# Performance work log

Hardware: AMD Instinct MI355X
Metric: run time of the kernel (lower is better)

Reference implementation:

```python
import jax, jax.numpy as jnp
import numpy as np

B = 262144          # batch
D = 128             # in_dim == out_dim
BS = 16             # block size
K = 8               # number of blocks
RANK = 4            # low-rank blocks' rank
DENSE = np.array([0, 3, 6])   # block ids with mode 'dense'
DIAG = np.array([1, 4, 7])    # block ids with mode 'diagonal'
LR = np.array([2, 5])         # block ids with mode 'lowrank'
EPS = 1e-8


def setup_inputs() -> dict:
    key = jax.random.key(0)
    k1, k2, k3, k4, k5 = jax.random.split(key, 5)
    x = jax.random.normal(k1, (B, D), dtype=jnp.float32)
    # dense blocks: torch init is identity (d_in==d_out); add noise so math is non-trivial
    W_dense = jnp.eye(BS, dtype=jnp.float32)[None] + 0.1 * jax.random.normal(k2, (len(DENSE), BS, BS), dtype=jnp.float32)
    # diagonal blocks: torch init is ones; perturb slightly
    s_diag = 1.0 + 0.1 * jax.random.normal(k3, (len(DIAG), BS), dtype=jnp.float32)
    # lowrank blocks: xavier-uniform-like scale
    lim = float(np.sqrt(6.0 / (BS + RANK)))
    U = jax.random.uniform(k4, (len(LR), BS, RANK), dtype=jnp.float32, minval=-lim, maxval=lim)
    V = jax.random.uniform(k5, (len(LR), BS, RANK), dtype=jnp.float32, minval=-lim, maxval=lim)
    return {"x": x, "W_dense": W_dense, "s_diag": s_diag, "U": U, "V": V}


def reference(x, W_dense, s_diag, U, V):
    # blocks are contiguous [16*j, 16*(j+1)), so gather == reshape to [B, K, BS]
    x3 = x.reshape(B, K, BS)
    # dense blocks: torch Linear y = x @ W.T, W is [d_out, d_in]
    yd = jnp.einsum('bkd,kod->bko', x3[:, DENSE], W_dense)
    # diagonal blocks: elementwise scale
    yg = x3[:, DIAG] * s_diag
    # lowrank blocks: x @ V @ U.T
    yl = jnp.einsum('bkr,kor->bko', jnp.einsum('bkd,kdr->bkr', x3[:, LR], V), U)
    y = jnp.zeros_like(x3).at[:, DENSE].set(yd).at[:, DIAG].set(yg).at[:, LR].set(yl)
    y = y.reshape(B, D)
    # l2 normalize (normalize=True)
    norm = jnp.linalg.norm(y, axis=-1, keepdims=True)
    return y / (norm + EPS)
```

## Files before the change

kernel.cpp:

```cpp
#include <hip/hip_runtime.h>

#define BATCH   262144
#define DDIM    128
#define GRID    2048
#define NITER   8

__global__ __launch_bounds__(256, 3) void bdla_kernel(
    const float* __restrict__ x,
    const float* __restrict__ Wd,
    const float* __restrict__ sd,
    const float* __restrict__ U,
    const float* __restrict__ V,
    float* __restrict__ out)
{
    __shared__ float lds[1072];
    const int tid = threadIdx.x;
    for (int i = tid; i < 768; i += 256) lds[i] = Wd[i];
    if (tid < 48)  lds[768 + tid] = sd[tid];
    if (tid < 128) lds[816 + tid] = U[tid];
    if (tid < 128) lds[944 + tid] = V[tid];
    __syncthreads();

    const int lane   = tid & 63;
    const int lane32 = lane & 31;
    const int half   = lane >> 5;
    const int j      = lane32 >> 2;
    const int sub    = lane32 & 3;
    const int mode   = j % 3;
    const int k      = j / 3;

    float A[4][16];
    if (mode == 0) {
        const float* w = &lds[k * 256];
#pragma unroll
        for (int oo = 0; oo < 4; ++oo) {
            const int o = sub * 4 + oo;
#pragma unroll
            for (int m = 0; m < 4; ++m)
#pragma unroll
                for (int c = 0; c < 4; ++c)
                    A[oo][m * 4 + c] = w[o * 16 + ((sub ^ m) * 4 + c)];
        }
    } else if (mode == 1) {
        const float* s = &lds[768 + k * 16];
#pragma unroll
        for (int oo = 0; oo < 4; ++oo)
#pragma unroll
            for (int m = 0; m < 4; ++m)
#pragma unroll
                for (int c = 0; c < 4; ++c)
                    A[oo][m * 4 + c] = (m == 0 && c == oo) ? s[sub * 4 + oo] : 0.0f;
    } else {
        const float* u = &lds[816 + k * 64];
        const float* v = &lds[944 + k * 64];
#pragma unroll
        for (int oo = 0; oo < 4; ++oo) {
            const int o = sub * 4 + oo;
#pragma unroll
            for (int m = 0; m < 4; ++m)
#pragma unroll
                for (int c = 0; c < 4; ++c) {
                    const int d = (sub ^ m) * 4 + c;
                    float acc = 0.0f;
#pragma unroll
                    for (int r = 0; r < 4; ++r)
                        acc += u[o * 4 + r] * v[d * 4 + r];
                    A[oo][m * 4 + c] = acc;
                }
        }
    }

#pragma unroll
    for (int oo = 0; oo < 4; ++oo)
#pragma unroll
        for (int t = 0; t < 16; ++t)
            asm volatile("" : "+v"(A[oo][t]));

    const int gw = blockIdx.x * 4 + (tid >> 6);
    const float* xbase = x   + (size_t)(gw * 4 + half) * DDIM + lane32 * 4;
    float*       obase = out + (size_t)(gw * 4 + half) * DDIM + lane32 * 4;
    const size_t istep = (size_t)(GRID * 4 * 4) * DDIM;

    float4 a0 = *(const float4*)(xbase);
    float4 b0 = *(const float4*)(xbase + 2 * DDIM);
    float4 a1 = *(const float4*)(xbase + istep);
    float4 b1 = *(const float4*)(xbase + istep + 2 * DDIM);

#pragma unroll
    for (int it = 0; it < NITER; ++it) {
        float4 a2, b2;
        if (it + 2 < NITER) {
            a2 = *(const float4*)(xbase + (size_t)(it + 2) * istep);
            b2 = *(const float4*)(xbase + (size_t)(it + 2) * istep + 2 * DDIM);
        }

        float ga[16], gb[16];
        ga[0] = a0.x; ga[1] = a0.y; ga[2] = a0.z; ga[3] = a0.w;
        gb[0] = b0.x; gb[1] = b0.y; gb[2] = b0.z; gb[3] = b0.w;
#pragma unroll
        for (int m = 1; m < 4; ++m) {
            ga[m * 4 + 0] = __shfl_xor(a0.x, m);
            ga[m * 4 + 1] = __shfl_xor(a0.y, m);
            ga[m * 4 + 2] = __shfl_xor(a0.z, m);
            ga[m * 4 + 3] = __shfl_xor(a0.w, m);
            gb[m * 4 + 0] = __shfl_xor(b0.x, m);
            gb[m * 4 + 1] = __shfl_xor(b0.y, m);
            gb[m * 4 + 2] = __shfl_xor(b0.z, m);
            gb[m * 4 + 3] = __shfl_xor(b0.w, m);
        }

        float ya0 = 0.f, ya1 = 0.f, ya2 = 0.f, ya3 = 0.f;
        float yb0 = 0.f, yb1 = 0.f, yb2 = 0.f, yb3 = 0.f;
#pragma unroll
        for (int t = 0; t < 16; ++t) {
            ya0 = fmaf(A[0][t], ga[t], ya0);
            ya1 = fmaf(A[1][t], ga[t], ya1);
            ya2 = fmaf(A[2][t], ga[t], ya2);
            ya3 = fmaf(A[3][t], ga[t], ya3);
            yb0 = fmaf(A[0][t], gb[t], yb0);
            yb1 = fmaf(A[1][t], gb[t], yb1);
            yb2 = fmaf(A[2][t], gb[t], yb2);
            yb3 = fmaf(A[3][t], gb[t], yb3);
        }

        float ssa = ya0 * ya0 + ya1 * ya1 + ya2 * ya2 + ya3 * ya3;
        float ssb = yb0 * yb0 + yb1 * yb1 + yb2 * yb2 + yb3 * yb3;
#pragma unroll
        for (int m = 1; m < 32; m <<= 1) {
            ssa += __shfl_xor(ssa, m);
            ssb += __shfl_xor(ssb, m);
        }
        const float inva = 1.0f / (sqrtf(ssa) + 1e-8f);
        const float invb = 1.0f / (sqrtf(ssb) + 1e-8f);

        float4 yva, yvb;
        yva.x = ya0 * inva; yva.y = ya1 * inva; yva.z = ya2 * inva; yva.w = ya3 * inva;
        yvb.x = yb0 * invb; yvb.y = yb1 * invb; yvb.z = yb2 * invb; yvb.w = yb3 * invb;
        *(float4*)(obase + (size_t)it * istep)            = yva;
        *(float4*)(obase + (size_t)it * istep + 2 * DDIM) = yvb;

        a0 = a1; b0 = b1; a1 = a2; b1 = b2;
    }
}

extern "C" void kernel_launch(void* const* d_in, const int* in_sizes, int n_in,
                              void* d_out, int out_size, void* d_ws, size_t ws_size,
                              hipStream_t stream) {
    const float* x  = (const float*)d_in[0];
    const float* Wd = (const float*)d_in[1];
    const float* sd = (const float*)d_in[2];
    const float* U  = (const float*)d_in[3];
    const float* V  = (const float*)d_in[4];
    float* out = (float*)d_out;
    (void)in_sizes; (void)n_in; (void)out_size; (void)d_ws; (void)ws_size;

    dim3 grid(GRID), block(256);
    hipLaunchKernelGGL(bdla_kernel, grid, block, 0, stream, x, Wd, sd, U, V, out);
}
```

Before: 241.0 us.

## Use DPP/swizzle lane exchanges, packed FMA, and nontemporal stores

Replaces the __shfl_xor calls (ds_bpermute through LDS hardware) with DPP quad permutes for the 4-lane gathers, and with DPP plus ds_swizzle for the 32-lane norm reduction. The per-row matvec now uses 2-wide float vectors so the compiler can emit packed FMA instructions. Output stores become nontemporal to avoid polluting the cache on this streaming, memory-bound kernel. The risks are that the packed layout raises register pressure and that the lane-exchange control constants may not match the original xor pattern.

```diff
diff --git a/kernel.cpp b/kernel.cpp
--- a/kernel.cpp
+++ b/kernel.cpp
@@ -4,6 +4,19 @@
 #define DDIM    128
 #define GRID    2048
 #define NITER   8
+
+typedef float v2f __attribute__((ext_vector_type(2)));
+typedef float v4f __attribute__((ext_vector_type(4)));
+
+template<int CTRL>
+__device__ __forceinline__ float qperm(float v) {
+    return __int_as_float(__builtin_amdgcn_update_dpp(
+        0, __float_as_int(v), CTRL, 0xF, 0xF, true));
+}
+template<int PAT>
+__device__ __forceinline__ float swz(float v) {
+    return __int_as_float(__builtin_amdgcn_ds_swizzle(__float_as_int(v), PAT));
+}
 
 __global__ __launch_bounds__(256, 3) void bdla_kernel(
     const float* __restrict__ x,
@@ -76,68 +89,69 @@
         for (int t = 0; t < 16; ++t)
             asm volatile("" : "+v"(A[oo][t]));
 
+    v2f A01[16], A23[16];
+#pragma unroll
+    for (int t = 0; t < 16; ++t) {
+        A01[t] = v2f{A[0][t], A[1][t]};
+        A23[t] = v2f{A[2][t], A[3][t]};
+    }
+
     const int gw = blockIdx.x * 4 + (tid >> 6);
     const float* xbase = x   + (size_t)(gw * 4 + half) * DDIM + lane32 * 4;
     float*       obase = out + (size_t)(gw * 4 + half) * DDIM + lane32 * 4;
     const size_t istep = (size_t)(GRID * 4 * 4) * DDIM;
 
-    float4 a0 = *(const float4*)(xbase);
-    float4 b0 = *(const float4*)(xbase + 2 * DDIM);
-    float4 a1 = *(const float4*)(xbase + istep);
-    float4 b1 = *(const float4*)(xbase + istep + 2 * DDIM);
+    auto rowcompute = [&](v4f r) -> v4f {
+        float g[16];
+        g[0] = r.x; g[1] = r.y; g[2] = r.z; g[3] = r.w;
+        g[4]  = qperm<0xB1>(r.x); g[5]  = qperm<0xB1>(r.y);
+        g[6]  = qperm<0xB1>(r.z); g[7]  = qperm<0xB1>(r.w);
+        g[8]  = qperm<0x4E>(r.x); g[9]  = qperm<0x4E>(r.y);
+        g[10] = qperm<0x4E>(r.z); g[11] = qperm<0x4E>(r.w);
+        g[12] = qperm<0x1B>(r.x); g[13] = qperm<0x1B>(r.y);
+        g[14] = qperm<0x1B>(r.z); g[15] = qperm<0x1B>(r.w);
+
+        v2f acc01 = v2f{0.f, 0.f}, acc23 = v2f{0.f, 0.f};
+#pragma unroll
+        for (int t = 0; t < 16; ++t) {
+            const v2f gg = v2f{g[t], g[t]};
+            acc01 += A01[t] * gg;
+            acc23 += A23[t] * gg;
+        }
+
+        float ss = acc01.x * acc01.x + acc01.y * acc01.y
+                 + acc23.x * acc23.x + acc23.y * acc23.y;
+        ss += qperm<0xB1>(ss);
+        ss += qperm<0x4E>(ss);
+        ss += swz<0x101F>(ss);
+        ss += swz<0x201F>(ss);
+        ss += swz<0x401F>(ss);
+        const float inv = 1.0f / (sqrtf(ss) + 1e-8f);
+
+        v4f y;
+        y.x = acc01.x * inv; y.y = acc01.y * inv;
+        y.z = acc23.x * inv; y.w = acc23.y * inv;
+        return y;
+    };
+
+    v4f a0 = *(const v4f*)(xbase);
+    v4f b0 = *(const v4f*)(xbase + 2 * DDIM);
+    v4f a1 = *(const v4f*)(xbase + istep);
+    v4f b1 = *(const v4f*)(xbase + istep + 2 * DDIM);
 
 #pragma unroll
     for (int it = 0; it < NITER; ++it) {
-        float4 a2, b2;
+        v4f a2, b2;
         if (it + 2 < NITER) {
-            a2 = *(const float4*)(xbase + (size_t)(it + 2) * istep);
-            b2 = *(const float4*)(xbase + (size_t)(it + 2) * istep + 2 * DDIM);
+            a2 = *(const v4f*)(xbase + (size_t)(it + 2) * istep);
+            b2 = *(const v4f*)(xbase + (size_t)(it + 2) * istep + 2 * DDIM);
         }
 
-        float ga[16], gb[16];
-        ga[0] = a0.x; ga[1] = a0.y; ga[2] = a0.z; ga[3] = a0.w;
-        gb[0] = b0.x; gb[1] = b0.y; gb[2] = b0.z; gb[3] = b0.w;
-#pragma unroll
-        for (int m = 1; m < 4; ++m) {
-            ga[m * 4 + 0] = __shfl_xor(a0.x, m);
-            ga[m * 4 + 1] = __shfl_xor(a0.y, m);
-            ga[m * 4 + 2] = __shfl_xor(a0.z, m);
-            ga[m * 4 + 3] = __shfl_xor(a0.w, m);
-            gb[m * 4 + 0] = __shfl_xor(b0.x, m);
-            gb[m * 4 + 1] = __shfl_xor(b0.y, m);
-            gb[m * 4 + 2] = __shfl_xor(b0.z, m);
-            gb[m * 4 + 3] = __shfl_xor(b0.w, m);
-        }
+        const v4f ya = rowcompute(a0);
+        const v4f yb = rowcompute(b0);
 
-        float ya0 = 0.f, ya1 = 0.f, ya2 = 0.f, ya3 = 0.f;
-        float yb0 = 0.f, yb1 = 0.f, yb2 = 0.f, yb3 = 0.f;
-#pragma unroll
-        for (int t = 0; t < 16; ++t) {
-            ya0 = fmaf(A[0][t], ga[t], ya0);
-            ya1 = fmaf(A[1][t], ga[t], ya1);
-            ya2 = fmaf(A[2][t], ga[t], ya2);
-            ya3 = fmaf(A[3][t], ga[t], ya3);
-            yb0 = fmaf(A[0][t], gb[t], yb0);
-            yb1 = fmaf(A[1][t], gb[t], yb1);
-            yb2 = fmaf(A[2][t], gb[t], yb2);
-            yb3 = fmaf(A[3][t], gb[t], yb3);
-        }
-
-        float ssa = ya0 * ya0 + ya1 * ya1 + ya2 * ya2 + ya3 * ya3;
-        float ssb = yb0 * yb0 + yb1 * yb1 + yb2 * yb2 + yb3 * yb3;
-#pragma unroll
-        for (int m = 1; m < 32; m <<= 1) {
-            ssa += __shfl_xor(ssa, m);
-            ssb += __shfl_xor(ssb, m);
-        }
-        const float inva = 1.0f / (sqrtf(ssa) + 1e-8f);
-        const float invb = 1.0f / (sqrtf(ssb) + 1e-8f);
-
-        float4 yva, yvb;
-        yva.x = ya0 * inva; yva.y = ya1 * inva; yva.z = ya2 * inva; yva.w = ya3 * inva;
-        yvb.x = yb0 * invb; yvb.y = yb1 * invb; yvb.z = yb2 * invb; yvb.w = yb3 * invb;
-        *(float4*)(obase + (size_t)it * istep)            = yva;
-        *(float4*)(obase + (size_t)it * istep + 2 * DDIM) = yvb;
+        __builtin_nontemporal_store(ya, (v4f*)(obase + (size_t)it * istep));
+        __builtin_nontemporal_store(yb, (v4f*)(obase + (size_t)it * istep + 2 * DDIM));
 
         a0 = a1; b0 = b1; a1 = a2; b1 = b2;
     }
```

Result: no change. 243.1 us (+0.9%).
